# Kernel tuning notes

Hardware: AMD Instinct MI355X
Metric: run time of the kernel (lower is better)

The kernel has to match this reference:

```python
import jax, jax.numpy as jnp
import numpy as np

EMBED_DIM = 1024
NB_HEADS = 16
HEAD_DIM = EMBED_DIM // NB_HEADS


def setup_inputs() -> dict:
    key = jax.random.key(0)
    ks = jax.random.split(key, 5)
    B, N, D = 4, 2048, EMBED_DIM
    scale = 1.0 / np.sqrt(D)
    return {
        "x": jax.random.normal(ks[0], (B, N, D), dtype=jnp.float32),
        "qkv_w": jax.random.normal(ks[1], (3 * D, D), dtype=jnp.float32) * scale,
        "qkv_b": jax.random.normal(ks[2], (3 * D,), dtype=jnp.float32) * 0.02,
        "proj_w": jax.random.normal(ks[3], (D, D), dtype=jnp.float32) * scale,
        "proj_b": jax.random.normal(ks[4], (D,), dtype=jnp.float32) * 0.02,
    }


def reference(x, qkv_w, qkv_b, proj_w, proj_b):
    B, N, D = x.shape
    H, Hd = NB_HEADS, HEAD_DIM
    # qkv projection: torch Linear => x @ W.T + b
    qkv = x @ qkv_w.T + qkv_b                       # [B, N, 3D]
    qkv = qkv.reshape(B, N, 3, H, Hd)
    q = jnp.transpose(qkv[:, :, 0], (0, 2, 1, 3))   # [B, H, N, Hd]
    k = jnp.transpose(qkv[:, :, 1], (0, 2, 1, 3))
    v = jnp.transpose(qkv[:, :, 2], (0, 2, 1, 3))
    scores = jnp.einsum("bhnd,bhmd->bhnm", q, k) * (Hd ** -0.5)  # [B,H,N,N]
    attn = jax.nn.softmax(scores, axis=-1)
    out = jnp.einsum("bhnm,bhmd->bhnd", attn, v)    # [B, H, N, Hd]
    out = jnp.transpose(out, (0, 2, 1, 3)).reshape(B, N, D)
    out = out @ proj_w.T + proj_b
    return out
```

## Files before the change

kernel.cpp:

```cpp
#include <hip/hip_runtime.h>


typedef __attribute__((ext_vector_type(8))) short bf16x8;
typedef __attribute__((ext_vector_type(4))) short s16x4;
typedef __attribute__((ext_vector_type(4))) float f32x4;
typedef __attribute__((ext_vector_type(16))) float f32x16;
typedef __attribute__((ext_vector_type(4))) unsigned u32x4;

#define LOG2E 1.44269504088896340736f

__device__ static inline short f2bf(float f) {
  unsigned u = __builtin_bit_cast(unsigned, f);
  unsigned r = (u + 0x7fffu + ((u >> 16) & 1u)) >> 16;
  return (short)r;
}
__device__ static inline unsigned cvtpk_bf16(float lo, float hi) {
  unsigned r;
  asm("v_cvt_pk_bf16_f32 %0, %1, %2" : "=v"(r) : "v"(lo), "v"(hi));
  return r;
}
__device__ static inline float exp2_hw(float x) {
#if __has_builtin(__builtin_amdgcn_exp2f)
  return __builtin_amdgcn_exp2f(x);
#else
  float r;
  asm("v_exp_f32 %0, %1" : "=v"(r) : "v"(x));
  return r;
#endif
}

__device__ static inline void gload_lds16(const void* g, void* l) {
  __builtin_amdgcn_global_load_lds(
      (const __attribute__((address_space(1))) void*)g,
      (__attribute__((address_space(3))) void*)l, 16, 0, 0);
}

__global__ void cvt_f32_bf16(const float* __restrict__ in, short* __restrict__ out, int n4) {
  int i = blockIdx.x * 256 + threadIdx.x;
  if (i < n4) {
    float4 v = ((const float4*)in)[i];
    s16x4 o4 = { f2bf(v.x), f2bf(v.y), f2bf(v.z), f2bf(v.w) };
    ((s16x4*)out)[i] = o4;
  }
}

template <int EPI>
__global__ __launch_bounds__(256, 2) void gemm_bt(
    const short* __restrict__ A, const short* __restrict__ Bm,
    const float* __restrict__ bias, int K,
    short* __restrict__ qo, short* __restrict__ ko, short* __restrict__ vto,
    float* __restrict__ outf) {
  __shared__ __align__(16) char smem[16384];
  char* As = smem;
  char* Bs = smem + 8192;
  const int tid = threadIdx.x, lane = tid & 63, w = tid >> 6;
  const int wm = w >> 1, wn = w & 1;
  const int bm = blockIdx.y, bn = blockIdx.x;

  f32x4 acc[4][4];
  const f32x4 z4 = {0.f, 0.f, 0.f, 0.f};
#pragma unroll
  for (int m = 0; m < 4; ++m)
#pragma unroll
    for (int n = 0; n < 4; ++n) acc[m][n] = z4;

  const short* Abase = A + (size_t)bm * 128 * K;
  const short* Bbase = Bm + (size_t)bn * 128 * K;

  for (int k0 = 0; k0 < K; k0 += 32) {
#pragma unroll
    for (int j = 0; j < 2; ++j) {
      int ia = w * 2 + j;
      int row = ia * 16 + (lane >> 2);
      int cl = (lane & 3) ^ (row & 3);
      gload_lds16(Abase + (size_t)row * K + k0 + cl * 8, As + ia * 1024);
      gload_lds16(Bbase + (size_t)row * K + k0 + cl * 8, Bs + ia * 1024);
    }
    __syncthreads();

    bf16x8 af[4], bf[4];
#pragma unroll
    for (int m = 0; m < 4; ++m) {
      int r = wm * 64 + m * 16 + (lane & 15);
      af[m] = *(const bf16x8*)(As + r * 64 + ((((lane >> 4)) ^ (r & 3)) << 4));
    }
#pragma unroll
    for (int n = 0; n < 4; ++n) {
      int r = wn * 64 + n * 16 + (lane & 15);
      bf[n] = *(const bf16x8*)(Bs + r * 64 + ((((lane >> 4)) ^ (r & 3)) << 4));
    }
#pragma unroll
    for (int m = 0; m < 4; ++m)
#pragma unroll
      for (int n = 0; n < 4; ++n)
        acc[m][n] = __builtin_amdgcn_mfma_f32_16x16x32_bf16(af[m], bf[n], acc[m][n], 0, 0, 0);
    __syncthreads();
  }

  if (EPI == 0) {
    const int which = bn >> 3;
    const int hh = ((bn & 7) << 1) | wn;
    const int bidx = bm >> 4;
    const size_t bh = (size_t)bidx * 16 + hh;
#pragma unroll
    for (int nf = 0; nf < 4; ++nf) {
      int dd = nf * 16 + (lane & 15);
      float bv = bias[bn * 128 + wn * 64 + dd];
#pragma unroll
      for (int m = 0; m < 4; ++m) {
        int nr0 = (bm & 15) * 128 + wm * 64 + m * 16 + ((lane >> 4) << 2);
        if (which == 2) {
          int nper = (nr0 & ~12) | ((nr0 & 4) << 1) | ((nr0 & 8) >> 1);
          s16x4 pk;
#pragma unroll
          for (int r = 0; r < 4; ++r) pk[r] = f2bf(acc[m][nf][r] + bv);
          *(s16x4*)(vto + (bh * 64 + dd) * 2048 + nper) = pk;
        } else if (which == 0) {
          short* dst = qo + (bh * 2048 + nr0) * 64 + dd;
#pragma unroll
          for (int r = 0; r < 4; ++r)
            dst[(size_t)r * 64] = f2bf((acc[m][nf][r] + bv) * (0.125f * LOG2E));
        } else {
          short* dst = ko + (bh * 2048 + nr0) * 64 + dd;
#pragma unroll
          for (int r = 0; r < 4; ++r) dst[(size_t)r * 64] = f2bf(acc[m][nf][r] + bv);
        }
      }
    }
  } else {
#pragma unroll
    for (int nf = 0; nf < 4; ++nf) {
      int gn = bn * 128 + wn * 64 + nf * 16 + (lane & 15);
      float bv = bias[gn];
#pragma unroll
      for (int m = 0; m < 4; ++m) {
        int gm0 = bm * 128 + wm * 64 + m * 16 + ((lane >> 4) << 2);
        float* dst = outf + (size_t)gm0 * 1024 + gn;
#pragma unroll
        for (int r = 0; r < 4; ++r) dst[(size_t)r * 1024] = acc[m][nf][r] + bv;
      }
    }
  }
}

#define BUILD_PF2(d0, d1, sv)                                                  \
  {                                                                            \
    u32x4 w0_ = {cvtpk_bf16(sv[0], sv[1]), cvtpk_bf16(sv[2], sv[3]),           \
                 cvtpk_bf16(sv[4], sv[5]), cvtpk_bf16(sv[6], sv[7])};          \
    d0 = __builtin_bit_cast(bf16x8, w0_);                                      \
    u32x4 w1_ = {cvtpk_bf16(sv[8], sv[9]), cvtpk_bf16(sv[10], sv[11]),         \
                 cvtpk_bf16(sv[12], sv[13]), cvtpk_bf16(sv[14], sv[15])};      \
    d1 = __builtin_bit_cast(bf16x8, w1_);                                      \
  }

__global__ __launch_bounds__(256, 3) void attn_kernel(
    const short* __restrict__ q, const short* __restrict__ kk,
    const short* __restrict__ vt, short* __restrict__ ao) {
  __shared__ __align__(16) char smem[32768];
  const int tid = threadIdx.x, lane = tid & 63, w = tid >> 6;
  const int r31 = lane & 31, h = lane >> 5;
  const int id = blockIdx.x;
  const int xcd = id & 7, p = id >> 3;
  const int bh = xcd * 8 + (p >> 4);
  const int qblk = p & 15;
  const int q0 = qblk * 128 + w * 32;

  const short* qptr = q + ((size_t)bh * 2048 + q0 + r31) * 64 + h * 8;
  const short* kgl = kk + (size_t)bh * 2048 * 64;
  const short* vgl = vt + (size_t)bh * 64 * 2048;

  const int srow = w * 16 + (lane >> 3);
  const int scol = ((lane & 7) * 8) ^ ((lane >> 3) << 3);
  const int ldst = w * 2048;

  bf16x8 qf[4];
#pragma unroll
  for (int dk = 0; dk < 4; ++dk) qf[dk] = *(const bf16x8*)(qptr + dk * 16);

  f32x16 o0, o1;
#pragma unroll
  for (int e = 0; e < 16; ++e) { o0[e] = 0.f; o1[e] = 0.f; }
  float ls[4];
#pragma unroll
  for (int e = 0; e < 4; ++e) ls[e] = 0.f;

#pragma unroll
  for (int j = 0; j < 2; ++j) {
    gload_lds16(kgl + (size_t)(srow + j * 8) * 64 + scol, smem + ldst + j * 1024);
    gload_lds16(vgl + (size_t)(srow + j * 8) * 2048 + scol, smem + 8192 + ldst + j * 1024);
  }
  __syncthreads();

  int cur = 0;
  for (int t = 0; t < 2048; t += 64) {
    const char* Kb = smem + cur * 16384;
    const char* Vb = smem + cur * 16384 + 8192;

    if (t + 64 < 2048) {
      char* nb = (char*)smem + (cur ^ 1) * 16384;
#pragma unroll
      for (int j = 0; j < 2; ++j) {
        gload_lds16(kgl + (size_t)(t + 64 + srow + j * 8) * 64 + scol, nb + ldst + j * 1024);
        gload_lds16(vgl + (size_t)(srow + j * 8) * 2048 + (t + 64) + scol, nb + 8192 + ldst + j * 1024);
      }
    }

    bf16x8 kf0[4], kf1[4];
#pragma unroll
    for (int dk = 0; dk < 4; ++dk) {
      int cb = (dk * 32 + h * 16) ^ ((r31 & 7) << 4);
      kf0[dk] = *(const bf16x8*)(Kb + r31 * 128 + cb);
      kf1[dk] = *(const bf16x8*)(Kb + (32 + r31) * 128 + cb);
    }

    f32x16 s0, s1;
#pragma unroll
    for (int e = 0; e < 16; ++e) { s0[e] = 0.f; s1[e] = 0.f; }
#pragma unroll
    for (int dk = 0; dk < 4; ++dk) {
      s0 = __builtin_amdgcn_mfma_f32_32x32x16_bf16(kf0[dk], qf[dk], s0, 0, 0, 0);
      s1 = __builtin_amdgcn_mfma_f32_32x32x16_bf16(kf1[dk], qf[dk], s1, 0, 0, 0);
    }

#pragma unroll
    for (int e = 0; e < 16; ++e) {
      s0[e] = exp2_hw(s0[e]);
      s1[e] = exp2_hw(s1[e]);
    }
#pragma unroll
    for (int e = 0; e < 4; ++e) {
      float t0 = (s0[e] + s0[e + 4]) + (s0[e + 8] + s0[e + 12]);
      float t1 = (s1[e] + s1[e + 4]) + (s1[e + 8] + s1[e + 12]);
      ls[e] += t0 + t1;
    }

    bf16x8 pf0, pf1, pf2, pf3;
    BUILD_PF2(pf0, pf1, s0);
    BUILD_PF2(pf2, pf3, s1);

    {
      bf16x8 v00, v10, v01, v11;
      int cb0 = (0 * 32 + h * 16) ^ ((r31 & 7) << 4);
      int cb1 = (1 * 32 + h * 16) ^ ((r31 & 7) << 4);
      v00 = *(const bf16x8*)(Vb + r31 * 128 + cb0);
      v10 = *(const bf16x8*)(Vb + (32 + r31) * 128 + cb0);
      v01 = *(const bf16x8*)(Vb + r31 * 128 + cb1);
      v11 = *(const bf16x8*)(Vb + (32 + r31) * 128 + cb1);
      o0 = __builtin_amdgcn_mfma_f32_32x32x16_bf16(v00, pf0, o0, 0, 0, 0);
      o1 = __builtin_amdgcn_mfma_f32_32x32x16_bf16(v10, pf0, o1, 0, 0, 0);
      o0 = __builtin_amdgcn_mfma_f32_32x32x16_bf16(v01, pf1, o0, 0, 0, 0);
      o1 = __builtin_amdgcn_mfma_f32_32x32x16_bf16(v11, pf1, o1, 0, 0, 0);
    }
    {
      bf16x8 v02, v12, v03, v13;
      int cb2 = (2 * 32 + h * 16) ^ ((r31 & 7) << 4);
      int cb3 = (3 * 32 + h * 16) ^ ((r31 & 7) << 4);
      v02 = *(const bf16x8*)(Vb + r31 * 128 + cb2);
      v12 = *(const bf16x8*)(Vb + (32 + r31) * 128 + cb2);
      v03 = *(const bf16x8*)(Vb + r31 * 128 + cb3);
      v13 = *(const bf16x8*)(Vb + (32 + r31) * 128 + cb3);
      o0 = __builtin_amdgcn_mfma_f32_32x32x16_bf16(v02, pf2, o0, 0, 0, 0);
      o1 = __builtin_amdgcn_mfma_f32_32x32x16_bf16(v12, pf2, o1, 0, 0, 0);
      o0 = __builtin_amdgcn_mfma_f32_32x32x16_bf16(v03, pf3, o0, 0, 0, 0);
      o1 = __builtin_amdgcn_mfma_f32_32x32x16_bf16(v13, pf3, o1, 0, 0, 0);
    }

    __syncthreads();
    cur ^= 1;
  }

  float lsum = (ls[0] + ls[1]) + (ls[2] + ls[3]);
  lsum += __shfl_xor(lsum, 32);

  const int b = bh >> 4, hd = bh & 15;
  float inv = 1.f / lsum;
  short* orow = ao + ((size_t)b * 2048 + q0 + r31) * 1024 + hd * 64;
#pragma unroll
  for (int s2 = 0; s2 < 4; ++s2) {
    s16x4 pk0, pk1;
#pragma unroll
    for (int r = 0; r < 4; ++r) {
      pk0[r] = f2bf(o0[4 * s2 + r] * inv);
      pk1[r] = f2bf(o1[4 * s2 + r] * inv);
    }
    *(s16x4*)(orow + 8 * s2 + 4 * h) = pk0;
    *(s16x4*)(orow + 32 + 8 * s2 + 4 * h) = pk1;
  }
}

extern "C" void kernel_launch(void* const* d_in, const int* in_sizes, int n_in,
                              void* d_out, int out_size, void* d_ws, size_t ws_size,
                              hipStream_t stream) {
  const float* x = (const float*)d_in[0];
  const float* qkv_w = (const float*)d_in[1];
  const float* qkv_b = (const float*)d_in[2];
  const float* proj_w = (const float*)d_in[3];
  const float* proj_b = (const float*)d_in[4];
  float* out = (float*)d_out;

  char* ws = (char*)d_ws;
  short* xb    = (short*)(ws + 0);
  short* wqkv  = (short*)(ws + 16777216);
  short* wproj = (short*)(ws + 23068672);
  short* qb    = (short*)(ws + 25165824);
  short* kb    = (short*)(ws + 41943040);
  short* vtb   = (short*)(ws + 58720256);
  short* aob   = (short*)(ws + 75497472);

  cvt_f32_bf16<<<8192, 256, 0, stream>>>(x, xb, 2097152);
  cvt_f32_bf16<<<3072, 256, 0, stream>>>(qkv_w, wqkv, 786432);
  cvt_f32_bf16<<<1024, 256, 0, stream>>>(proj_w, wproj, 262144);

  gemm_bt<0><<<dim3(24, 64), 256, 0, stream>>>(xb, wqkv, qkv_b, 1024, qb, kb, vtb, nullptr);
  attn_kernel<<<1024, 256, 0, stream>>>(qb, kb, vtb, aob);
  gemm_bt<1><<<dim3(8, 64), 256, 0, stream>>>(aob, wproj, proj_b, 1024, nullptr, nullptr, nullptr, out);
}
```

Baseline: 198.9 us.

## Add 256x256 double-buffered pipelined QKV GEMM kernel with 512 threads

Replaces the generic 128x128 QKV projection GEMM with a dedicated kernel that uses 256x256 block tiles, 8 waves and 128 KB of LDS split into two buffers. Global-to-LDS loads for the next K tile are issued per phase and overlapped with MFMA work, using explicit barriers, waitcnt and setprio. The larger tile is meant to raise data reuse and hide load latency. In exchange it needs more LDS and registers per block, and the grid shrinks to 384 blocks, which may leave CUs unevenly loaded.

```diff
diff --git a/kernel.cpp b/kernel.cpp
--- a/kernel.cpp
+++ b/kernel.cpp
@@ -44,11 +44,141 @@
   }
 }
 
+__global__ __launch_bounds__(512, 2) void gemm_qkv(
+    const short* __restrict__ A, const short* __restrict__ Bm,
+    const float* __restrict__ bias,
+    short* __restrict__ qo, short* __restrict__ ko, short* __restrict__ vto) {
+  __shared__ __align__(16) char smem[131072];
+  const int tid = threadIdx.x, lane = tid & 63, w = tid >> 6;
+  const int wm = w >> 2, wn = w & 3;
+  const int bn = blockIdx.x, bm = blockIdx.y;
+  const int fr = lane & 15;
+  const int cb0 = ((((lane >> 4))     ^ (lane & 7)) << 4);
+  const int cb1 = ((((lane >> 4)) + 4 ^ (lane & 7)) << 4);
+
+  char* ldsA0 = smem;
+  char* ldsB0 = smem + 32768;
+  char* ldsA1 = smem + 65536;
+  char* ldsB1 = smem + 98304;
+
+  const short* Ag = A + (size_t)(bm * 256) * 1024;
+  const short* Bg = Bm + (size_t)(bn * 256) * 1024;
+
+  auto STAGE = [&](const short* __restrict__ mg, int kt, int half, char* ldsmat) {
+#pragma unroll
+    for (int sw = 0; sw < 2; ++sw) {
+      int r = half * 128 + sw * 64 + w * 8 + (lane >> 3);
+      gload_lds16(mg + (size_t)r * 1024 + (kt & 15) * 64 + ((lane & 7) ^ (lane >> 3)) * 8,
+                  ldsmat + (half * 128 + sw * 64 + w * 8) * 128);
+    }
+  };
+
+  f32x4 acc[8][4];
+  const f32x4 z4 = {0.f, 0.f, 0.f, 0.f};
+#pragma unroll
+  for (int i = 0; i < 8; ++i)
+#pragma unroll
+    for (int j = 0; j < 4; ++j) acc[i][j] = z4;
+
+  bf16x8 a[4][2], b[2][2];
+
+  STAGE(Ag, 0, 0, ldsA0);
+  STAGE(Ag, 0, 1, ldsA0);
+  STAGE(Bg, 0, 0, ldsB0);
+  STAGE(Bg, 0, 1, ldsB0);
+  STAGE(Ag, 1, 0, ldsA1);
+  asm volatile("s_waitcnt vmcnt(2)" ::: "memory");
+  __builtin_amdgcn_s_barrier();
+
+#define PHASE(BUF, MH, NH, RDA, SG, SLDS, STILE, SHALF, W2)                    \
+  {                                                                            \
+    const char* Ab_ = smem + (BUF) * 65536;                                    \
+    const char* Bb_ = Ab_ + 32768;                                             \
+    if (RDA) {                                                                 \
+      _Pragma("unroll")                                                        \
+      for (int mf = 0; mf < 4; ++mf) {                                         \
+        const char* ar = Ab_ + (wm * 128 + (MH) * 64 + mf * 16 + fr) * 128;    \
+        a[mf][0] = *(const bf16x8*)(ar + cb0);                                 \
+        a[mf][1] = *(const bf16x8*)(ar + cb1);                                 \
+      }                                                                        \
+    }                                                                          \
+    _Pragma("unroll")                                                          \
+    for (int nf = 0; nf < 2; ++nf) {                                           \
+      const char* br = Bb_ + (wn * 64 + (NH) * 32 + nf * 16 + fr) * 128;       \
+      b[nf][0] = *(const bf16x8*)(br + cb0);                                   \
+      b[nf][1] = *(const bf16x8*)(br + cb1);                                   \
+    }                                                                          \
+    STAGE(SG, STILE, SHALF, SLDS);                                             \
+    __builtin_amdgcn_s_barrier();                                              \
+    __builtin_amdgcn_sched_barrier(0);                                         \
+    __builtin_amdgcn_s_setprio(1);                                             \
+    _Pragma("unroll")                                                          \
+    for (int mf = 0; mf < 4; ++mf) {                                           \
+      _Pragma("unroll")                                                        \
+      for (int nf = 0; nf < 2; ++nf) {                                         \
+        acc[(MH)*4 + mf][(NH)*2 + nf] = __builtin_amdgcn_mfma_f32_16x16x32_bf16( \
+            a[mf][0], b[nf][0], acc[(MH)*4 + mf][(NH)*2 + nf], 0, 0, 0);       \
+        acc[(MH)*4 + mf][(NH)*2 + nf] = __builtin_amdgcn_mfma_f32_16x16x32_bf16( \
+            a[mf][1], b[nf][1], acc[(MH)*4 + mf][(NH)*2 + nf], 0, 0, 0);       \
+      }                                                                        \
+    }                                                                          \
+    __builtin_amdgcn_s_setprio(0);                                             \
+    if (W2) asm volatile("s_waitcnt vmcnt(2)" ::: "memory");                   \
+    __builtin_amdgcn_s_barrier();                                              \
+    __builtin_amdgcn_sched_barrier(0);                                         \
+  }
+
+  for (int j = 0; j < 8; ++j) {
+    const int t0 = 2 * j;
+    PHASE(0, 0, 0, true,  Ag, ldsA1, t0 + 1, 1, false);
+    PHASE(0, 0, 1, false, Bg, ldsB1, t0 + 1, 0, false);
+    PHASE(0, 1, 0, true,  Bg, ldsB1, t0 + 1, 1, false);
+    PHASE(0, 1, 1, false, Ag, ldsA0, t0 + 2, 0, true);
+    PHASE(1, 0, 0, true,  Ag, ldsA0, t0 + 2, 1, false);
+    PHASE(1, 0, 1, false, Bg, ldsB0, t0 + 2, 0, false);
+    PHASE(1, 1, 0, true,  Bg, ldsB0, t0 + 2, 1, false);
+    PHASE(1, 1, 1, false, Ag, ldsA1, t0 + 3, 0, true);
+  }
+#undef PHASE
+
+  asm volatile("s_waitcnt vmcnt(0)" ::: "memory");
+
+  const int which = bn >> 2;
+  const int head = (bn & 3) * 4 + wn;
+  const int batch = bm >> 3;
+  const size_t bh = (size_t)batch * 16 + head;
+  const int rbase = (bm & 7) * 256 + wm * 128 + ((lane >> 4) << 2);
+#pragma unroll
+  for (int nf16 = 0; nf16 < 4; ++nf16) {
+    const int dd = nf16 * 16 + fr;
+    const float bv = bias[bn * 256 + wn * 64 + dd];
+#pragma unroll
+    for (int mf = 0; mf < 8; ++mf) {
+      const int nr0 = rbase + mf * 16;
+      if (which == 2) {
+        int nper = (nr0 & ~12) | ((nr0 & 4) << 1) | ((nr0 & 8) >> 1);
+        s16x4 pk;
+#pragma unroll
+        for (int r = 0; r < 4; ++r) pk[r] = f2bf(acc[mf][nf16][r] + bv);
+        *(s16x4*)(vto + (bh * 64 + dd) * 2048 + nper) = pk;
+      } else if (which == 0) {
+        short* dst = qo + (bh * 2048 + nr0) * 64 + dd;
+#pragma unroll
+        for (int r = 0; r < 4; ++r)
+          dst[(size_t)r * 64] = f2bf((acc[mf][nf16][r] + bv) * (0.125f * LOG2E));
+      } else {
+        short* dst = ko + (bh * 2048 + nr0) * 64 + dd;
+#pragma unroll
+        for (int r = 0; r < 4; ++r) dst[(size_t)r * 64] = f2bf(acc[mf][nf16][r] + bv);
+      }
+    }
+  }
+}
+
 template <int EPI>
 __global__ __launch_bounds__(256, 2) void gemm_bt(
     const short* __restrict__ A, const short* __restrict__ Bm,
     const float* __restrict__ bias, int K,
-    short* __restrict__ qo, short* __restrict__ ko, short* __restrict__ vto,
     float* __restrict__ outf) {
   __shared__ __align__(16) char smem[16384];
   char* As = smem;
@@ -97,48 +227,16 @@
     __syncthreads();
   }
 
-  if (EPI == 0) {
-    const int which = bn >> 3;
-    const int hh = ((bn & 7) << 1) | wn;
-    const int bidx = bm >> 4;
-    const size_t bh = (size_t)bidx * 16 + hh;
-#pragma unroll
-    for (int nf = 0; nf < 4; ++nf) {
-      int dd = nf * 16 + (lane & 15);
-      float bv = bias[bn * 128 + wn * 64 + dd];
-#pragma unroll
-      for (int m = 0; m < 4; ++m) {
-        int nr0 = (bm & 15) * 128 + wm * 64 + m * 16 + ((lane >> 4) << 2);
-        if (which == 2) {
-          int nper = (nr0 & ~12) | ((nr0 & 4) << 1) | ((nr0 & 8) >> 1);
-          s16x4 pk;
-#pragma unroll
-          for (int r = 0; r < 4; ++r) pk[r] = f2bf(acc[m][nf][r] + bv);
-          *(s16x4*)(vto + (bh * 64 + dd) * 2048 + nper) = pk;
-        } else if (which == 0) {
-          short* dst = qo + (bh * 2048 + nr0) * 64 + dd;
-#pragma unroll
-          for (int r = 0; r < 4; ++r)
-            dst[(size_t)r * 64] = f2bf((acc[m][nf][r] + bv) * (0.125f * LOG2E));
-        } else {
-          short* dst = ko + (bh * 2048 + nr0) * 64 + dd;
-#pragma unroll
-          for (int r = 0; r < 4; ++r) dst[(size_t)r * 64] = f2bf(acc[m][nf][r] + bv);
-        }
-      }
-    }
-  } else {
-#pragma unroll
-    for (int nf = 0; nf < 4; ++nf) {
-      int gn = bn * 128 + wn * 64 + nf * 16 + (lane & 15);
-      float bv = bias[gn];
-#pragma unroll
-      for (int m = 0; m < 4; ++m) {
-        int gm0 = bm * 128 + wm * 64 + m * 16 + ((lane >> 4) << 2);
-        float* dst = outf + (size_t)gm0 * 1024 + gn;
-#pragma unroll
-        for (int r = 0; r < 4; ++r) dst[(size_t)r * 1024] = acc[m][nf][r] + bv;
-      }
+#pragma unroll
+  for (int nf = 0; nf < 4; ++nf) {
+    int gn = bn * 128 + wn * 64 + nf * 16 + (lane & 15);
+    float bv = bias[gn];
+#pragma unroll
+    for (int m = 0; m < 4; ++m) {
+      int gm0 = bm * 128 + wm * 64 + m * 16 + ((lane >> 4) << 2);
+      float* dst = outf + (size_t)gm0 * 1024 + gn;
+#pragma unroll
+      for (int r = 0; r < 4; ++r) dst[(size_t)r * 1024] = acc[m][nf][r] + bv;
     }
   }
 }
@@ -311,7 +409,7 @@
   cvt_f32_bf16<<<3072, 256, 0, stream>>>(qkv_w, wqkv, 786432);
   cvt_f32_bf16<<<1024, 256, 0, stream>>>(proj_w, wproj, 262144);
 
-  gemm_bt<0><<<dim3(24, 64), 256, 0, stream>>>(xb, wqkv, qkv_b, 1024, qb, kb, vtb, nullptr);
+  gemm_qkv<<<dim3(12, 32), 512, 0, stream>>>(xb, wqkv, qkv_b, qb, kb, vtb);
   attn_kernel<<<1024, 256, 0, stream>>>(qb, kb, vtb, aob);
-  gemm_bt<1><<<dim3(8, 64), 256, 0, stream>>>(aob, wproj, proj_b, 1024, nullptr, nullptr, nullptr, out);
-}
+  gemm_bt<1><<<dim3(8, 64), 256, 0, stream>>>(aob, wproj, proj_b, 1024, out);
+}
```

Result: no change. 199.3 us (+0.2%).
